# Performance work log

Hardware: AMD Instinct MI355X
Metric: run time of the kernel (lower is better)

Reference implementation:

```python
import jax, jax.numpy as jnp
import numpy as np


def setup_inputs() -> dict:
    key = jax.random.key(0)
    k1, k2, k3 = jax.random.split(key, 3)
    B, S, H = 32, 2048, 1024
    lstm_output = jax.random.normal(k1, (B, S, H), dtype=jnp.float32)
    final_hidden = jax.random.normal(k2, (B, H), dtype=jnp.float32)
    # nn.Linear(2H, 1): weight [1, 2H], bias [1]
    W = jax.random.normal(k3, (1, 2 * H), dtype=jnp.float32) * (1.0 / np.sqrt(2 * H))
    b = jnp.zeros((1,), dtype=jnp.float32)
    return {"lstm_output": lstm_output, "final_hidden": final_hidden, "W": W, "b": b}


def reference(lstm_output, final_hidden, W, b):
    # Equivalent to cat([lstm_output, repeat(final_hidden)]) @ W.T + b,
    # but split W to avoid materializing the [B, S, 2H] concat.
    H = lstm_output.shape[-1]
    w1 = W[0, :H]   # applies to lstm_output
    w2 = W[0, H:]   # applies to final_hidden
    # scores: [B, S]
    scores = jnp.einsum('bsh,h->bs', lstm_output, w1) \
           + (final_hidden @ w2)[:, None] + b[0]
    attn_weights = jax.nn.softmax(scores, axis=1)              # [B, S]
    context_vector = jnp.einsum('bs,bsh->bh', attn_weights, lstm_output)
    return context_vector, attn_weights
```

## Files before the change

### kernel.cpp

```cpp
#include <hip/hip_runtime.h>


#define B_ 32
#define S_ 2048
#define H_ 1024
#define ROWS 16
#define WAVES_PER_BATCH (S_ / ROWS)
#define NWAVE (B_ * WAVES_PER_BATCH)
#define NBLK (NWAVE / 4)

__global__ __launch_bounds__(256) void fused_pass(
    const float* __restrict__ lstm, const float* __restrict__ W,
    float* __restrict__ esc, float* __restrict__ part, float* __restrict__ lpart)
{
    const int tid  = threadIdx.x;
    const int wave = tid >> 6;
    const int lane = tid & 63;
    const int gw   = blockIdx.x * 4 + wave;
    const int b    = gw >> 7;
    const int s0   = (gw & 127) * ROWS;

    float4 w[4];
#pragma unroll
    for (int q = 0; q < 4; ++q)
        w[q] = *(const float4*)(W + q * 256 + lane * 4);

    float4 acc[4];
#pragma unroll
    for (int q = 0; q < 4; ++q) acc[q] = make_float4(0.f, 0.f, 0.f, 0.f);
    float l = 0.f;

    const float* base = lstm + ((size_t)b * S_ + s0) * H_ + lane * 4;

#pragma unroll
    for (int t = 0; t < ROWS / 4; ++t) {
        const float* rb = base + (size_t)(t * 4) * H_;
        float4 v[4][4];
#pragma unroll
        for (int r = 0; r < 4; ++r)
#pragma unroll
            for (int q = 0; q < 4; ++q)
                v[r][q] = *(const float4*)(rb + (size_t)r * H_ + q * 256);

        float d[4];
#pragma unroll
        for (int r = 0; r < 4; ++r) {
            float s = v[r][0].x * w[0].x + v[r][0].y * w[0].y
                    + v[r][0].z * w[0].z + v[r][0].w * w[0].w;
#pragma unroll
            for (int q = 1; q < 4; ++q)
                s += v[r][q].x * w[q].x + v[r][q].y * w[q].y
                   + v[r][q].z * w[q].z + v[r][q].w * w[q].w;
            d[r] = s;
        }
#pragma unroll
        for (int off = 32; off >= 1; off >>= 1) {
#pragma unroll
            for (int r = 0; r < 4; ++r)
                d[r] += __shfl_xor(d[r], off, 64);
        }
        float e[4];
#pragma unroll
        for (int r = 0; r < 4; ++r) e[r] = __expf(d[r]);
        if (lane == 0)
            *(float4*)(esc + (size_t)b * S_ + s0 + t * 4) =
                make_float4(e[0], e[1], e[2], e[3]);
        l += (e[0] + e[1]) + (e[2] + e[3]);
#pragma unroll
        for (int r = 0; r < 4; ++r) {
#pragma unroll
            for (int q = 0; q < 4; ++q) {
                acc[q].x = fmaf(e[r], v[r][q].x, acc[q].x);
                acc[q].y = fmaf(e[r], v[r][q].y, acc[q].y);
                acc[q].z = fmaf(e[r], v[r][q].z, acc[q].z);
                acc[q].w = fmaf(e[r], v[r][q].w, acc[q].w);
            }
        }
    }

    float* pp = part + (size_t)gw * H_ + lane * 4;
#pragma unroll
    for (int q = 0; q < 4; ++q) *(float4*)(pp + q * 256) = acc[q];
    if (lane == 0) lpart[gw] = l;
}

__global__ __launch_bounds__(256) void combine_k(
    const float* __restrict__ part, const float* __restrict__ lpart,
    float* __restrict__ ctx_out, float* __restrict__ Lws)
{
    const int b = blockIdx.x;
    const int h = blockIdx.y * 256 + threadIdx.x;
    float L = 0.f;
#pragma unroll 16
    for (int j = 0; j < WAVES_PER_BATCH; ++j)
        L += lpart[b * WAVES_PER_BATCH + j];
    float sum = 0.f;
#pragma unroll 8
    for (int j = 0; j < WAVES_PER_BATCH; ++j)
        sum += part[(size_t)(b * WAVES_PER_BATCH + j) * H_ + h];
    ctx_out[(size_t)b * H_ + h] = sum / L;
    if (blockIdx.y == 0 && threadIdx.x == 0) Lws[b] = L;
}

__global__ __launch_bounds__(256) void attn_k(
    const float* __restrict__ esc, const float* __restrict__ Lws,
    float* __restrict__ attn_out)
{
    const int i = blockIdx.x * 256 + threadIdx.x;
    const int b = i >> 9;
    const float invL = 1.0f / Lws[b];
    const float4 e = ((const float4*)esc)[i];
    float4 o;
    o.x = e.x * invL; o.y = e.y * invL; o.z = e.z * invL; o.w = e.w * invL;
    ((float4*)attn_out)[i] = o;
}

extern "C" void kernel_launch(void* const* d_in, const int* in_sizes, int n_in,
                              void* d_out, int out_size, void* d_ws, size_t ws_size,
                              hipStream_t stream)
{
    const float* lstm = (const float*)d_in[0];
    const float* W    = (const float*)d_in[2];

    float* out  = (float*)d_out;
    float* ctx  = out;
    float* attn = out + B_ * H_;

    float* ws    = (float*)d_ws;
    float* esc   = ws;
    float* part  = ws + (size_t)B_ * S_;
    float* lpart = part + (size_t)NWAVE * H_;
    float* Lws   = lpart + NWAVE;

    fused_pass<<<NBLK, 256, 0, stream>>>(lstm, W, esc, part, lpart);
    combine_k<<<dim3(B_, H_ / 256), 256, 0, stream>>>(part, lpart, ctx, Lws);
    attn_k<<<(B_ * S_) / (4 * 256), 256, 0, stream>>>(esc, Lws, attn);
}
```

Measured before the change: 372.3 us.

## Double-buffer row loads and reduce partials per block in shared memory

The main loop now processes two rows per step and prefetches the next pair into a second register buffer while the current pair is computed, replacing the four-row load-then-compute batches. The four waves of each block sum their context partials and exp-sums in LDS before writing, which cuts the partial buffer and the work of the combine kernel by a factor of four. The attention kernel recomputes the per-batch sum from block partials instead of reading a value written by the combine kernel. This adds 16KB of LDS per block and a block barrier, which could lower occupancy.

```diff
diff --git a/kernel.cpp b/kernel.cpp
--- a/kernel.cpp
+++ b/kernel.cpp
@@ -5,13 +5,15 @@
 #define S_ 2048
 #define H_ 1024
 #define ROWS 16
+#define BATCH2 (ROWS / 2)
 #define WAVES_PER_BATCH (S_ / ROWS)
 #define NWAVE (B_ * WAVES_PER_BATCH)
 #define NBLK (NWAVE / 4)
+#define BLK_PER_B (NBLK / B_)
 
 __global__ __launch_bounds__(256) void fused_pass(
     const float* __restrict__ lstm, const float* __restrict__ W,
-    float* __restrict__ esc, float* __restrict__ part, float* __restrict__ lpart)
+    float* __restrict__ esc, float* __restrict__ part, float* __restrict__ lblk)
 {
     const int tid  = threadIdx.x;
     const int wave = tid >> 6;
@@ -32,83 +34,102 @@
 
     const float* base = lstm + ((size_t)b * S_ + s0) * H_ + lane * 4;
 
+    float4 va[2][4], vb[2][4];
 #pragma unroll
-    for (int t = 0; t < ROWS / 4; ++t) {
-        const float* rb = base + (size_t)(t * 4) * H_;
-        float4 v[4][4];
+    for (int r = 0; r < 2; ++r)
 #pragma unroll
-        for (int r = 0; r < 4; ++r)
+        for (int q = 0; q < 4; ++q)
+            va[r][q] = *(const float4*)(base + (size_t)r * H_ + q * 256);
+
 #pragma unroll
-            for (int q = 0; q < 4; ++q)
-                v[r][q] = *(const float4*)(rb + (size_t)r * H_ + q * 256);
-
-        float d[4];
+    for (int t = 0; t < BATCH2; ++t) {
+        float4 (*cur)[4] = (t & 1) ? vb : va;
+        float4 (*nxt)[4] = (t & 1) ? va : vb;
+        if (t + 1 < BATCH2) {
+            const float* nb = base + (size_t)((t + 1) * 2) * H_;
 #pragma unroll
-        for (int r = 0; r < 4; ++r) {
-            float s = v[r][0].x * w[0].x + v[r][0].y * w[0].y
-                    + v[r][0].z * w[0].z + v[r][0].w * w[0].w;
+            for (int r = 0; r < 2; ++r)
 #pragma unroll
-            for (int q = 1; q < 4; ++q)
-                s += v[r][q].x * w[q].x + v[r][q].y * w[q].y
-                   + v[r][q].z * w[q].z + v[r][q].w * w[q].w;
-            d[r] = s;
+                for (int q = 0; q < 4; ++q)
+                    nxt[r][q] = *(const float4*)(nb + (size_t)r * H_ + q * 256);
+        }
+        float d0 = cur[0][0].x * w[0].x + cur[0][0].y * w[0].y
+                 + cur[0][0].z * w[0].z + cur[0][0].w * w[0].w;
+        float d1 = cur[1][0].x * w[0].x + cur[1][0].y * w[0].y
+                 + cur[1][0].z * w[0].z + cur[1][0].w * w[0].w;
+#pragma unroll
+        for (int q = 1; q < 4; ++q) {
+            d0 += cur[0][q].x * w[q].x + cur[0][q].y * w[q].y
+                + cur[0][q].z * w[q].z + cur[0][q].w * w[q].w;
+            d1 += cur[1][q].x * w[q].x + cur[1][q].y * w[q].y
+                + cur[1][q].z * w[q].z + cur[1][q].w * w[q].w;
         }
 #pragma unroll
         for (int off = 32; off >= 1; off >>= 1) {
+            d0 += __shfl_xor(d0, off, 64);
+            d1 += __shfl_xor(d1, off, 64);
+        }
+        const float e0 = __expf(d0), e1 = __expf(d1);
+        if (lane == 0)
+            *(float2*)(esc + (size_t)b * S_ + s0 + t * 2) = make_float2(e0, e1);
+        l += e0 + e1;
 #pragma unroll
-            for (int r = 0; r < 4; ++r)
-                d[r] += __shfl_xor(d[r], off, 64);
-        }
-        float e[4];
-#pragma unroll
-        for (int r = 0; r < 4; ++r) e[r] = __expf(d[r]);
-        if (lane == 0)
-            *(float4*)(esc + (size_t)b * S_ + s0 + t * 4) =
-                make_float4(e[0], e[1], e[2], e[3]);
-        l += (e[0] + e[1]) + (e[2] + e[3]);
-#pragma unroll
-        for (int r = 0; r < 4; ++r) {
-#pragma unroll
-            for (int q = 0; q < 4; ++q) {
-                acc[q].x = fmaf(e[r], v[r][q].x, acc[q].x);
-                acc[q].y = fmaf(e[r], v[r][q].y, acc[q].y);
-                acc[q].z = fmaf(e[r], v[r][q].z, acc[q].z);
-                acc[q].w = fmaf(e[r], v[r][q].w, acc[q].w);
-            }
+        for (int q = 0; q < 4; ++q) {
+            acc[q].x = fmaf(e0, cur[0][q].x, fmaf(e1, cur[1][q].x, acc[q].x));
+            acc[q].y = fmaf(e0, cur[0][q].y, fmaf(e1, cur[1][q].y, acc[q].y));
+            acc[q].z = fmaf(e0, cur[0][q].z, fmaf(e1, cur[1][q].z, acc[q].z));
+            acc[q].w = fmaf(e0, cur[0][q].w, fmaf(e1, cur[1][q].w, acc[q].w));
         }
     }
 
-    float* pp = part + (size_t)gw * H_ + lane * 4;
+    __shared__ float red[4 * H_];
+    __shared__ float lred[4];
+    float* my = red + wave * H_ + lane * 4;
 #pragma unroll
-    for (int q = 0; q < 4; ++q) *(float4*)(pp + q * 256) = acc[q];
-    if (lane == 0) lpart[gw] = l;
+    for (int q = 0; q < 4; ++q) *(float4*)(my + q * 256) = acc[q];
+    if (lane == 0) lred[wave] = l;
+    __syncthreads();
+
+    const int h = tid * 4;
+    float4 s0v = *(const float4*)(red + 0 * H_ + h);
+    float4 s1v = *(const float4*)(red + 1 * H_ + h);
+    float4 s2v = *(const float4*)(red + 2 * H_ + h);
+    float4 s3v = *(const float4*)(red + 3 * H_ + h);
+    float4 sm;
+    sm.x = (s0v.x + s1v.x) + (s2v.x + s3v.x);
+    sm.y = (s0v.y + s1v.y) + (s2v.y + s3v.y);
+    sm.z = (s0v.z + s1v.z) + (s2v.z + s3v.z);
+    sm.w = (s0v.w + s1v.w) + (s2v.w + s3v.w);
+    *(float4*)(part + (size_t)blockIdx.x * H_ + h) = sm;
+    if (tid == 0) lblk[blockIdx.x] = (lred[0] + lred[1]) + (lred[2] + lred[3]);
 }
 
 __global__ __launch_bounds__(256) void combine_k(
-    const float* __restrict__ part, const float* __restrict__ lpart,
-    float* __restrict__ ctx_out, float* __restrict__ Lws)
+    const float* __restrict__ part, const float* __restrict__ lblk,
+    float* __restrict__ ctx_out)
 {
     const int b = blockIdx.x;
     const int h = blockIdx.y * 256 + threadIdx.x;
     float L = 0.f;
-#pragma unroll 16
-    for (int j = 0; j < WAVES_PER_BATCH; ++j)
-        L += lpart[b * WAVES_PER_BATCH + j];
+#pragma unroll
+    for (int j = 0; j < BLK_PER_B; ++j) L += lblk[b * BLK_PER_B + j];
     float sum = 0.f;
-#pragma unroll 8
-    for (int j = 0; j < WAVES_PER_BATCH; ++j)
-        sum += part[(size_t)(b * WAVES_PER_BATCH + j) * H_ + h];
+#pragma unroll
+    for (int j = 0; j < BLK_PER_B; ++j)
+        sum += part[(size_t)(b * BLK_PER_B + j) * H_ + h];
     ctx_out[(size_t)b * H_ + h] = sum / L;
-    if (blockIdx.y == 0 && threadIdx.x == 0) Lws[b] = L;
 }
 
 __global__ __launch_bounds__(256) void attn_k(
-    const float* __restrict__ esc, const float* __restrict__ Lws,
+    const float* __restrict__ esc, const float* __restrict__ lblk,
     float* __restrict__ attn_out)
 {
     const int i = blockIdx.x * 256 + threadIdx.x;
     const int b = i >> 9;
-    const float invL = 1.0f / Lws[b];
+    float L = 0.f;
+#pragma unroll
+    for (int j = 0; j < BLK_PER_B; ++j) L += lblk[b * BLK_PER_B + j];
+    const float invL = 1.0f / L;
     const float4 e = ((const float4*)esc)[i];
     float4 o;
     o.x = e.x * invL; o.y = e.y * invL; o.z = e.z * invL; o.w = e.w * invL;
@@ -126,13 +147,12 @@
     float* ctx  = out;
     float* attn = out + B_ * H_;
 
-    float* ws    = (float*)d_ws;
-    float* esc   = ws;
-    float* part  = ws + (size_t)B_ * S_;
-    float* lpart = part + (size_t)NWAVE * H_;
-    float* Lws   = lpart + NWAVE;
+    float* ws   = (float*)d_ws;
+    float* esc  = ws;
+    float* part = ws + (size_t)B_ * S_;
+    float* lblk = part + (size_t)NBLK * H_;
 
-    fused_pass<<<NBLK, 256, 0, stream>>>(lstm, W, esc, part, lpart);
-    combine_k<<<dim3(B_, H_ / 256), 256, 0, stream>>>(part, lpart, ctx, Lws);
-    attn_k<<<(B_ * S_) / (4 * 256), 256, 0, stream>>>(esc, Lws, attn);
+    fused_pass<<<NBLK, 256, 0, stream>>>(lstm, W, esc, part, lblk);
+    combine_k<<<dim3(B_, H_ / 256), 256, 0, stream>>>(part, lblk, ctx);
+    attn_k<<<(B_ * S_) / (4 * 256), 256, 0, stream>>>(esc, lblk, attn);
 }
```

Result: no change. 365.7 us (-1.8%).
